# Optimization experiments

Measured on AMD Instinct MI355X. Metric: run time of the kernel, lower is better.

Reference implementation:

```python
import jax, jax.numpy as jnp
import numpy as np

B, V = 1024, 16            # batch, n_variables
NH, SHARE = 32, 4          # n_base_heads, n_heads_sharing_slider
SH = NH // SHARE           # n_slider_heads = 8
D = 128                    # n_token_dim
KV = D * SH                # kv_size = 1024
H = 4096                   # n_hidden


def setup_inputs() -> dict:
    key = jax.random.key(0)
    ks = jax.random.split(key, 14)
    s = 0.02
    inp = {
        "prefix": jax.random.uniform(ks[0], (B, V), jnp.float32, -1.0, 1.0),
        # stacked per-variable key-encoder weights
        "kW1": jax.random.normal(ks[1], (V, KV), jnp.float32) * s,
        "kb1": jnp.zeros((V, KV), jnp.float32),
        "kW2": jax.random.normal(ks[2], (V, KV, H), jnp.float32) * s,
        "kb2": jnp.zeros((V, H), jnp.float32),
        "kW3": jax.random.normal(ks[3], (V, H, KV), jnp.float32) * s,
        "kb3": jnp.zeros((V, KV), jnp.float32),
        # stacked per-variable value-encoder weights
        "vW1": jax.random.normal(ks[4], (V, KV), jnp.float32) * s,
        "vb1": jnp.zeros((V, KV), jnp.float32),
        "vW2": jax.random.normal(ks[5], (V, KV, H), jnp.float32) * s,
        "vb2": jnp.zeros((V, H), jnp.float32),
        "vW3": jax.random.normal(ks[6], (V, H, KV), jnp.float32) * s,
        "vb3": jnp.zeros((V, KV), jnp.float32),
        "attention_factor": jnp.zeros((), jnp.float32),
    }
    return inp


def _mlp(x, W1, b1, W2, b2, W3, b3):
    # x: [B, V] scalar slider per variable; stacked tiny MLPs over V.
    h = jnp.tanh(x[:, :, None] * W1[None] + b1[None])            # [B,V,KV]
    h = jnp.tanh(jnp.einsum('bvk,vkh->bvh', h, W2) + b2[None])   # [B,V,H]
    return jnp.einsum('bvh,vhk->bvk', h, W3) + b3[None]          # [B,V,KV]


def _to_heads(x):
    # [B,V,KV] -> [B, n_base_heads, V, D] with repeat_interleave over slider heads
    x = x.reshape(B, V, SH, D)
    x = jnp.repeat(x, SHARE, axis=2)            # [B,V,NH,D]
    return jnp.transpose(x, (0, 2, 1, 3))       # [B,NH,V,D]


def reference(prefix, kW1, kb1, kW2, kb2, kW3, kb3,
              vW1, vb1, vW2, vb2, vW3, vb3, attention_factor):
    keys = _to_heads(_mlp(prefix, kW1, kb1, kW2, kb2, kW3, kb3))
    values = _to_heads(_mlp(prefix, vW1, vb1, vW2, vb2, vW3, vb3))
    return keys, values, attention_factor
```

## Files before the change

### kernel.cpp

```cpp
#include <hip/hip_runtime.h>
#include <hip/hip_bf16.h>
#include <cstdint>

#define B_   1024
#define V_   16
#define NH_  32
#define SH_  8
#define D_   128
#define KV_  1024
#define H_   4096

typedef __bf16 bf16;
typedef bf16  bf16x8 __attribute__((ext_vector_type(8)));
typedef float f32x2  __attribute__((ext_vector_type(2)));
typedef float f32x4  __attribute__((ext_vector_type(4)));

#define VMCNT(n) asm volatile("s_waitcnt vmcnt(" #n ")" ::: "memory")
#define LGKM0()  asm volatile("s_waitcnt lgkmcnt(0)" ::: "memory")

__device__ __forceinline__ void gl2lds16(const void* g, void* l) {
    __builtin_amdgcn_global_load_lds((const __attribute__((address_space(1))) void*)g,
                                     (__attribute__((address_space(3))) void*)l,
                                     16, 0, 0);
}

__global__ __launch_bounds__(256)
void h1_kernel(const float* __restrict__ prefix, const float* __restrict__ W1,
               const float* __restrict__ b1, bf16* __restrict__ h1)
{
    int gid = blockIdx.x * 256 + threadIdx.x;
    int k8  = gid & 127;
    int b   = (gid >> 7) & 1023;
    int v   = gid >> 17;
    float x = prefix[b * V_ + v];
    const float* wp = W1 + (size_t)v * KV_ + k8 * 8;
    const float* bp = b1 + (size_t)v * KV_ + k8 * 8;
    f32x4 w0 = *(const f32x4*)wp,       w1 = *(const f32x4*)(wp + 4);
    f32x4 q0 = *(const f32x4*)bp,       q1 = *(const f32x4*)(bp + 4);
    bf16x8 o;
#pragma unroll
    for (int j = 0; j < 4; ++j) o[j]     = (bf16)tanhf(fmaf(x, w0[j], q0[j]));
#pragma unroll
    for (int j = 0; j < 4; ++j) o[4 + j] = (bf16)tanhf(fmaf(x, w1[j], q1[j]));
    *(bf16x8*)(h1 + (size_t)gid * 8) = o;
}

template<int MODE, int KDIM, int NDIM>
__global__ __launch_bounds__(512)
void gemm_w(const bf16* __restrict__ A, const float* __restrict__ Bf,
            const float* __restrict__ bias,
            bf16* __restrict__ outB, float* __restrict__ outF)
{
    __shared__ __align__(16) char smem[98304];

    const int v  = blockIdx.z;
    const int m0 = blockIdx.y * 256;
    const int n0 = blockIdx.x * 128;
    const int t  = threadIdx.x;
    const int l  = t & 63;
    const int w  = t >> 6;
    const int wr = w >> 1;
    const int wc = w & 1;
    constexpr int NT = KDIM / 64;
    static_assert(NT >= 4 && (NT % 2) == 0, "NT must be even and >= 4");

    const bf16*  Av = A  + (size_t)v * 1024 * KDIM + (size_t)m0 * KDIM;
    const float* Bv = Bf + (size_t)v * KDIM * NDIM + n0;

    f32x4 acc[4][4];
#pragma unroll
    for (int i = 0; i < 4; ++i)
#pragma unroll
        for (int j = 0; j < 4; ++j) acc[i][j] = f32x4{0.f, 0.f, 0.f, 0.f};

    const float* bptr = Bv + (size_t)(w * 8) * NDIM + 2 * l;
    f32x2 brA[8], brB[8];

    auto loadBR = [&](int ktile, f32x2 (&bank)[8]) {
        const float* np = bptr + (size_t)ktile * 64 * NDIM;
#pragma unroll
        for (int j = 0; j < 8; ++j) bank[j] = *(const f32x2*)(np + (size_t)j * NDIM);
    };
    auto stageA = [&](int ktile, int ab) {
#pragma unroll
        for (int i = 0; i < 4; ++i) {
            const int off = t + i * 512;
            const int row = off >> 3;
            const int gc  = (off & 7) ^ ((row >> 1) & 7);
            gl2lds16(Av + (size_t)row * KDIM + ktile * 64 + gc * 8,
                     smem + (size_t)ab * 32768 + (size_t)off * 16);
        }
    };
    auto writeB = [&](f32x2 (&bank)[8], int bb) {
        bf16* bN = (bf16*)(smem + 65536 + (size_t)bb * 16384);
#pragma unroll
        for (int i = 0; i < 2; ++i) {
            bf16x8 pk;
#pragma unroll
            for (int jj = 0; jj < 8; ++jj) pk[jj] = (bf16)bank[jj][i];
            const int n  = 2 * l + i;
            const int ch = w ^ (l & 7);
            *(bf16x8*)(bN + n * 64 + ch * 8) = pk;
        }
    };
    auto mfmaStep = [&](int kt) {
        const bf16* aC = (const bf16*)(smem + (size_t)(kt & 1) * 32768);
        const bf16* bC = (const bf16*)(smem + 65536 + (size_t)(kt & 1) * 16384);
#pragma unroll
        for (int kk = 0; kk < 2; ++kk) {
            bf16x8 af[4], bfv[4];
#pragma unroll
            for (int f = 0; f < 4; ++f) {
                const int mr = wr * 64 + f * 16 + (l & 15);
                const int ca = (kk * 4 + (l >> 4)) ^ ((mr >> 1) & 7);
                af[f]  = *(const bf16x8*)(aC + mr * 64 + ca * 8);
                const int nr = wc * 64 + f * 16 + (l & 15);
                const int cb = (kk * 4 + (l >> 4)) ^ ((nr >> 1) & 7);
                bfv[f] = *(const bf16x8*)(bC + nr * 64 + cb * 8);
            }
#pragma unroll
            for (int fm = 0; fm < 4; ++fm)
#pragma unroll
                for (int fn = 0; fn < 4; ++fn)
                    acc[fm][fn] = __builtin_amdgcn_mfma_f32_16x16x32_bf16(
                        af[fm], bfv[fn], acc[fm][fn], 0, 0, 0);
        }
    };

    stageA(0, 0);
    loadBR(0, brA);
    loadBR(1, brB);
    VMCNT(8);
    writeB(brA, 0);
    LGKM0();
    __builtin_amdgcn_s_barrier();

    auto stepS = [&](int kt, f32x2 (&brIss)[8], f32x2 (&brUse)[8]) {
        stageA(kt + 1, (kt + 1) & 1);
        loadBR(kt + 2, brIss);
        mfmaStep(kt);
        VMCNT(12);
        writeB(brUse, (kt + 1) & 1);
        VMCNT(8);
        LGKM0();
        __builtin_amdgcn_s_barrier();
    };
    for (int kt = 0; kt + 3 < NT; kt += 2) {
        stepS(kt,     brA, brB);
        stepS(kt + 1, brB, brA);
    }
    {
        stageA(NT - 1, (NT - 1) & 1);
        mfmaStep(NT - 2);
        VMCNT(4);
        writeB(brB, (NT - 1) & 1);
        VMCNT(0);
        LGKM0();
        __builtin_amdgcn_s_barrier();
    }
    mfmaStep(NT - 1);

    const int rbase = (l >> 4) * 4;
    const int cbase = l & 15;
    if (MODE == 0) {
#pragma unroll
        for (int fn = 0; fn < 4; ++fn) {
            const int nc = n0 + wc * 64 + fn * 16 + cbase;
            const float bv = bias[(size_t)v * NDIM + nc];
#pragma unroll
            for (int fm = 0; fm < 4; ++fm)
#pragma unroll
                for (int j = 0; j < 4; ++j) {
                    const int mr = m0 + wr * 64 + fm * 16 + rbase + j;
                    outB[(size_t)v * 1024 * NDIM + (size_t)mr * NDIM + nc] =
                        (bf16)tanhf(acc[fm][fn][j] + bv);
                }
        }
    } else {
        __syncthreads();
        float* scr = (float*)(smem + (size_t)w * 8192);
        const int nb = n0 + wc * 64;
        const int sh = nb >> 7;
        const int db = nb & 127;
#pragma unroll
        for (int p = 0; p < 2; ++p) {
#pragma unroll
            for (int fm = 0; fm < 4; ++fm)
#pragma unroll
                for (int fq = 0; fq < 2; ++fq) {
                    const int fn = 2 * p + fq;
#pragma unroll
                    for (int j = 0; j < 4; ++j) {
                        const int r = fm * 16 + rbase + j;
                        const int c = fq * 16 + cbase;
                        scr[r * 32 + (c ^ (((r >> 2) & 1) << 4))] = acc[fm][fn][j];
                    }
                }
            const int c4   = (l & 7) * 4;
            const int colg = p * 32 + c4;
            f32x4 bv4;
#pragma unroll
            for (int q = 0; q < 4; ++q)
                bv4[q] = bias[(size_t)v * NDIM + nb + colg + q];
#pragma unroll
            for (int i = 0; i < 8; ++i) {
                const int r = i * 8 + (l >> 3);
                f32x4 val = *(const f32x4*)&scr[r * 32 + (c4 ^ (((r >> 2) & 1) << 4))];
#pragma unroll
                for (int q = 0; q < 4; ++q) val[q] += bv4[q];
                const int mr = m0 + wr * 64 + r;
                float* pp = outF + (size_t)mr * (NH_ * V_ * D_)
                                 + (size_t)(sh * 4) * (V_ * D_)
                                 + (size_t)v * D_ + db + colg;
                *(f32x4*)(pp)               = val;
                *(f32x4*)(pp + V_ * D_)     = val;
                *(f32x4*)(pp + 2 * V_ * D_) = val;
                *(f32x4*)(pp + 3 * V_ * D_) = val;
            }
        }
    }
}

__global__ void tail_kernel(const float* __restrict__ af, float* __restrict__ out)
{
    out[0] = af[0];
}

extern "C" void kernel_launch(void* const* d_in, const int* in_sizes, int n_in,
                              void* d_out, int out_size, void* d_ws, size_t ws_size,
                              hipStream_t stream)
{
    const float* prefix = (const float*)d_in[0];
    const float* W1[2]  = {(const float*)d_in[1], (const float*)d_in[7]};
    const float* b1[2]  = {(const float*)d_in[2], (const float*)d_in[8]};
    const float* W2[2]  = {(const float*)d_in[3], (const float*)d_in[9]};
    const float* b2[2]  = {(const float*)d_in[4], (const float*)d_in[10]};
    const float* W3[2]  = {(const float*)d_in[5], (const float*)d_in[11]};
    const float* b3[2]  = {(const float*)d_in[6], (const float*)d_in[12]};
    const float* afac   = (const float*)d_in[13];

    bf16* h1 = (bf16*)d_ws;
    bf16* h2 = (bf16*)((char*)d_ws + (size_t)33554432);
    float* outp = (float*)d_out;

    for (int m = 0; m < 2; ++m) {
        h1_kernel<<<8192, 256, 0, stream>>>(prefix, W1[m], b1[m], h1);
        gemm_w<0, 1024, 4096><<<dim3(32, 4, 16), 512, 0, stream>>>(
            h1, W2[m], b2[m], h2, nullptr);
        gemm_w<1, 4096, 1024><<<dim3(8, 4, 16), 512, 0, stream>>>(
            h2, W3[m], b3[m], nullptr, outp + (size_t)m * (B_ * NH_ * V_ * D_));
    }
    tail_kernel<<<1, 1, 0, stream>>>(afac, outp + (size_t)2 * B_ * NH_ * V_ * D_);
}
```

Measured before the change: 1.045 ms.

## Enlarge GEMM tile to 256x256 with XCD-aware block swizzle and simpler pipeline

Both per-variable GEMMs move from 256x128 to 256x256 output tiles. Each warp now computes 128x64 with 8x4 MFMA accumulators, which halves how often the fp32 weight matrix and the A tiles are re-read per output. Blocks are remapped with a chunked swizzle over the linear block id so neighbouring blocks land on the same XCD, aiming for better L2 reuse. The B-register prefetch drops from two banks issued two tiles ahead to a single bank one tile ahead. This raises register and LDS pressure (128 KB of shared memory) and leaves fewer blocks in flight.

```diff
diff --git a/kernel.cpp b/kernel.cpp
--- a/kernel.cpp
+++ b/kernel.cpp
@@ -47,39 +47,47 @@
 
 template<int MODE, int KDIM, int NDIM>
 __global__ __launch_bounds__(512)
-void gemm_w(const bf16* __restrict__ A, const float* __restrict__ Bf,
-            const float* __restrict__ bias,
-            bf16* __restrict__ outB, float* __restrict__ outF)
-{
-    __shared__ __align__(16) char smem[98304];
-
-    const int v  = blockIdx.z;
-    const int m0 = blockIdx.y * 256;
-    const int n0 = blockIdx.x * 128;
+void gemm_t2(const bf16* __restrict__ A, const float* __restrict__ Bf,
+             const float* __restrict__ bias,
+             bf16* __restrict__ outB, float* __restrict__ outF)
+{
+    __shared__ __align__(16) char smem[131072];
+
+    constexpr int NX  = NDIM / 256;
+    constexpr int NXY = NX * 4;
+    const int lin = blockIdx.x + NX * blockIdx.y + NXY * blockIdx.z;
+    constexpr int NWG = NXY * 16;
+    constexpr int CHK = NWG / 8;
+    const int swz = (lin & 7) * CHK + (lin >> 3);
+    const int v   = swz / NXY;
+    const int rem = swz - v * NXY;
+    const int m0  = (rem / NX) * 256;
+    const int n0  = (rem - (rem / NX) * NX) * 256;
+
     const int t  = threadIdx.x;
     const int l  = t & 63;
     const int w  = t >> 6;
-    const int wr = w >> 1;
-    const int wc = w & 1;
+    const int wr = w >> 2;
+    const int wc = w & 3;
     constexpr int NT = KDIM / 64;
-    static_assert(NT >= 4 && (NT % 2) == 0, "NT must be even and >= 4");
+    static_assert(NT >= 4, "NT >= 4");
 
     const bf16*  Av = A  + (size_t)v * 1024 * KDIM + (size_t)m0 * KDIM;
     const float* Bv = Bf + (size_t)v * KDIM * NDIM + n0;
 
-    f32x4 acc[4][4];
-#pragma unroll
-    for (int i = 0; i < 4; ++i)
+    f32x4 acc[8][4];
+#pragma unroll
+    for (int i = 0; i < 8; ++i)
 #pragma unroll
         for (int j = 0; j < 4; ++j) acc[i][j] = f32x4{0.f, 0.f, 0.f, 0.f};
 
-    const float* bptr = Bv + (size_t)(w * 8) * NDIM + 2 * l;
-    f32x2 brA[8], brB[8];
-
-    auto loadBR = [&](int ktile, f32x2 (&bank)[8]) {
+    const float* bptr = Bv + (size_t)((t >> 7) * 16) * NDIM + 2 * (t & 127);
+    f32x2 br[16];
+
+    auto loadBR = [&](int ktile) {
         const float* np = bptr + (size_t)ktile * 64 * NDIM;
 #pragma unroll
-        for (int j = 0; j < 8; ++j) bank[j] = *(const f32x2*)(np + (size_t)j * NDIM);
+        for (int j = 0; j < 16; ++j) br[j] = *(const f32x2*)(np + (size_t)j * NDIM);
     };
     auto stageA = [&](int ktile, int ab) {
 #pragma unroll
@@ -91,35 +99,40 @@
                      smem + (size_t)ab * 32768 + (size_t)off * 16);
         }
     };
-    auto writeB = [&](f32x2 (&bank)[8], int bb) {
-        bf16* bN = (bf16*)(smem + 65536 + (size_t)bb * 16384);
-#pragma unroll
-        for (int i = 0; i < 2; ++i) {
-            bf16x8 pk;
-#pragma unroll
-            for (int jj = 0; jj < 8; ++jj) pk[jj] = (bf16)bank[jj][i];
-            const int n  = 2 * l + i;
-            const int ch = w ^ (l & 7);
-            *(bf16x8*)(bN + n * 64 + ch * 8) = pk;
-        }
+    auto writeB = [&](int bb) {
+        bf16* bN = (bf16*)(smem + 65536 + (size_t)bb * 32768);
+#pragma unroll
+        for (int i = 0; i < 2; ++i)
+#pragma unroll
+            for (int h = 0; h < 2; ++h) {
+                bf16x8 pk;
+#pragma unroll
+                for (int jj = 0; jj < 8; ++jj) pk[jj] = (bf16)br[h * 8 + jj][i];
+                const int n  = 2 * (t & 127) + i;
+                const int ch = ((t >> 7) * 2 + h) ^ (t & 7);
+                *(bf16x8*)(bN + (size_t)n * 64 + ch * 8) = pk;
+            }
     };
     auto mfmaStep = [&](int kt) {
         const bf16* aC = (const bf16*)(smem + (size_t)(kt & 1) * 32768);
-        const bf16* bC = (const bf16*)(smem + 65536 + (size_t)(kt & 1) * 16384);
+        const bf16* bC = (const bf16*)(smem + 65536 + (size_t)(kt & 1) * 32768);
 #pragma unroll
         for (int kk = 0; kk < 2; ++kk) {
-            bf16x8 af[4], bfv[4];
+            bf16x8 af[8], bfv[4];
+#pragma unroll
+            for (int f = 0; f < 8; ++f) {
+                const int mr = wr * 128 + f * 16 + (l & 15);
+                const int ca = (kk * 4 + (l >> 4)) ^ ((mr >> 1) & 7);
+                af[f] = *(const bf16x8*)(aC + (size_t)mr * 64 + ca * 8);
+            }
 #pragma unroll
             for (int f = 0; f < 4; ++f) {
-                const int mr = wr * 64 + f * 16 + (l & 15);
-                const int ca = (kk * 4 + (l >> 4)) ^ ((mr >> 1) & 7);
-                af[f]  = *(const bf16x8*)(aC + mr * 64 + ca * 8);
                 const int nr = wc * 64 + f * 16 + (l & 15);
                 const int cb = (kk * 4 + (l >> 4)) ^ ((nr >> 1) & 7);
-                bfv[f] = *(const bf16x8*)(bC + nr * 64 + cb * 8);
-            }
-#pragma unroll
-            for (int fm = 0; fm < 4; ++fm)
+                bfv[f] = *(const bf16x8*)(bC + (size_t)nr * 64 + cb * 8);
+            }
+#pragma unroll
+            for (int fm = 0; fm < 8; ++fm)
 #pragma unroll
                 for (int fn = 0; fn < 4; ++fn)
                     acc[fm][fn] = __builtin_amdgcn_mfma_f32_16x16x32_bf16(
@@ -127,33 +140,20 @@
         }
     };
 
+    loadBR(0);
     stageA(0, 0);
-    loadBR(0, brA);
-    loadBR(1, brB);
-    VMCNT(8);
-    writeB(brA, 0);
+    VMCNT(4);
+    writeB(0);
+    VMCNT(0);
     LGKM0();
     __builtin_amdgcn_s_barrier();
 
-    auto stepS = [&](int kt, f32x2 (&brIss)[8], f32x2 (&brUse)[8]) {
+    for (int kt = 0; kt < NT - 1; ++kt) {
+        loadBR(kt + 1);
         stageA(kt + 1, (kt + 1) & 1);
-        loadBR(kt + 2, brIss);
         mfmaStep(kt);
-        VMCNT(12);
-        writeB(brUse, (kt + 1) & 1);
-        VMCNT(8);
-        LGKM0();
-        __builtin_amdgcn_s_barrier();
-    };
-    for (int kt = 0; kt + 3 < NT; kt += 2) {
-        stepS(kt,     brA, brB);
-        stepS(kt + 1, brB, brA);
-    }
-    {
-        stageA(NT - 1, (NT - 1) & 1);
-        mfmaStep(NT - 2);
         VMCNT(4);
-        writeB(brB, (NT - 1) & 1);
+        writeB((kt + 1) & 1);
         VMCNT(0);
         LGKM0();
         __builtin_amdgcn_s_barrier();
@@ -168,24 +168,24 @@
             const int nc = n0 + wc * 64 + fn * 16 + cbase;
             const float bv = bias[(size_t)v * NDIM + nc];
 #pragma unroll
-            for (int fm = 0; fm < 4; ++fm)
+            for (int fm = 0; fm < 8; ++fm)
 #pragma unroll
                 for (int j = 0; j < 4; ++j) {
-                    const int mr = m0 + wr * 64 + fm * 16 + rbase + j;
+                    const int mr = m0 + wr * 128 + fm * 16 + rbase + j;
                     outB[(size_t)v * 1024 * NDIM + (size_t)mr * NDIM + nc] =
                         (bf16)tanhf(acc[fm][fn][j] + bv);
                 }
         }
     } else {
         __syncthreads();
-        float* scr = (float*)(smem + (size_t)w * 8192);
+        float* scr = (float*)(smem + (size_t)w * 16384);
         const int nb = n0 + wc * 64;
         const int sh = nb >> 7;
         const int db = nb & 127;
 #pragma unroll
         for (int p = 0; p < 2; ++p) {
 #pragma unroll
-            for (int fm = 0; fm < 4; ++fm)
+            for (int fm = 0; fm < 8; ++fm)
 #pragma unroll
                 for (int fq = 0; fq < 2; ++fq) {
                     const int fn = 2 * p + fq;
@@ -203,12 +203,12 @@
             for (int q = 0; q < 4; ++q)
                 bv4[q] = bias[(size_t)v * NDIM + nb + colg + q];
 #pragma unroll
-            for (int i = 0; i < 8; ++i) {
+            for (int i = 0; i < 16; ++i) {
                 const int r = i * 8 + (l >> 3);
                 f32x4 val = *(const f32x4*)&scr[r * 32 + (c4 ^ (((r >> 2) & 1) << 4))];
 #pragma unroll
                 for (int q = 0; q < 4; ++q) val[q] += bv4[q];
-                const int mr = m0 + wr * 64 + r;
+                const int mr = m0 + wr * 128 + r;
                 float* pp = outF + (size_t)mr * (NH_ * V_ * D_)
                                  + (size_t)(sh * 4) * (V_ * D_)
                                  + (size_t)v * D_ + db + colg;
@@ -245,9 +245,9 @@
 
     for (int m = 0; m < 2; ++m) {
         h1_kernel<<<8192, 256, 0, stream>>>(prefix, W1[m], b1[m], h1);
-        gemm_w<0, 1024, 4096><<<dim3(32, 4, 16), 512, 0, stream>>>(
+        gemm_t2<0, 1024, 4096><<<dim3(16, 4, 16), 512, 0, stream>>>(
             h1, W2[m], b2[m], h2, nullptr);
-        gemm_w<1, 4096, 1024><<<dim3(8, 4, 16), 512, 0, stream>>>(
+        gemm_t2<1, 4096, 1024><<<dim3(4, 4, 16), 512, 0, stream>>>(
             h2, W3[m], b3[m], nullptr, outp + (size_t)m * (B_ * NH_ * V_ * D_));
     }
     tail_kernel<<<1, 1, 0, stream>>>(afac, outp + (size_t)2 * B_ * NH_ * V_ * D_);
```

New measurement: 913.4 us. 12.6% less time.
